# Performance work log

Measured on AMD Instinct MI355X. Metric: run time of the kernel, lower is better.

## Reference

```python
import jax, jax.numpy as jnp
import numpy as np

B, S, D = 2, 4096, 1024
H, HD = 16, 64
M = 512              # memseqlen == chunk size
L = 2 * M            # memory + chunk tokens
HID = 2816
EPS = 1e-5


def setup_inputs() -> dict:
    key = jax.random.key(0)
    ks = jax.random.split(key, 16)
    sc = 0.02
    return {
        "x": jax.random.normal(ks[0], (B, S, D), jnp.float32),
        "freqs_cos": jax.random.uniform(ks[1], (L, HD // 2), jnp.float32),
        "freqs_sin": jax.random.uniform(ks[2], (L, HD // 2), jnp.float32),
        "wq": jax.random.normal(ks[3], (D, D), jnp.float32) * sc,
        "wk": jax.random.normal(ks[4], (D, D), jnp.float32) * sc,
        "wv": jax.random.normal(ks[5], (D, D), jnp.float32) * sc,
        "wo": jax.random.normal(ks[6], (D, D), jnp.float32) * sc,
        "wm": jax.random.normal(ks[7], (D, D), jnp.float32) * sc,
        "wkm": jax.random.normal(ks[8], (D, D), jnp.float32) * sc,
        "wvm": jax.random.normal(ks[9], (D, D), jnp.float32) * sc,
        "w1": jax.random.normal(ks[10], (D, HID), jnp.float32) * sc,
        "w3": jax.random.normal(ks[11], (D, HID), jnp.float32) * sc,
        "w2": jax.random.normal(ks[12], (HID, D), jnp.float32) * sc,
        "ffn_norm_w": jnp.ones((D,), jnp.float32),
        "mem_norm_w": jnp.ones((D,), jnp.float32),
        "origin_mem": jnp.zeros((1, M, D), jnp.float32),
    }


def _rmsnorm(x, w):
    return x * jax.lax.rsqrt(jnp.mean(x * x, axis=-1, keepdims=True) + EPS) * w


def _rope(t, cos, sin):
    # t: (B, L, H, HD); cos/sin: (L, HD//2). Adjacent-pair complex rotation (llama2.c style).
    tr = t.reshape(*t.shape[:-1], HD // 2, 2)
    t_r, t_i = tr[..., 0], tr[..., 1]
    c = cos[None, :, None, :]
    s = sin[None, :, None, :]
    o_r = t_r * c - t_i * s
    o_i = t_r * s + t_i * c
    return jnp.stack([o_r, o_i], axis=-1).reshape(t.shape)


def reference(x, freqs_cos, freqs_sin, wq, wk, wv, wo, wm, wkm, wvm,
              w1, w2, w3, ffn_norm_w, mem_norm_w, origin_mem):
    bsz = x.shape[0]
    cos = freqs_cos[:L]
    sin = freqs_sin[:L]
    causal = jnp.tril(jnp.ones((L, L), dtype=bool))
    scale = 1.0 / jnp.sqrt(jnp.asarray(HD, x.dtype))

    def ffn(h):
        return (jax.nn.silu(h @ w1) * (h @ w3)) @ w2

    def step(om, subx):
        # token projections
        xq = (subx @ wq).reshape(bsz, M, H, HD)
        xk = (subx @ wk).reshape(bsz, M, H, HD)
        xv = (subx @ wv).reshape(bsz, M, H, HD)
        # memory glue: wm -> ffn residual -> rmsnorm
        om2 = om @ wm
        om2 = om2 + ffn(_rmsnorm(om2, ffn_norm_w))
        om2 = _rmsnorm(om2, mem_norm_w)
        # memory projections (source bug: mq is overwritten by mk; wqm unused)
        mk = (om2 @ wkm).reshape(bsz, M, H, HD)
        mv = (om2 @ wvm).reshape(bsz, M, H, HD)
        mq = mk
        q = jnp.concatenate([mq, xq], axis=1)  # (B, L, H, HD)
        k = jnp.concatenate([mk, xk], axis=1)
        v = jnp.concatenate([mv, xv], axis=1)
        q = _rope(q, cos, sin)
        k = _rope(k, cos, sin)
        # SDPA, causal over the concatenated length (n_rep == 1, repeat_kv is identity)
        qh = q.transpose(0, 2, 1, 3)
        kh = k.transpose(0, 2, 1, 3)
        vh = v.transpose(0, 2, 1, 3)
        scores = jnp.einsum('bhqd,bhkd->bhqk', qh, kh) * scale
        scores = jnp.where(causal, scores, jnp.finfo(scores.dtype).min)
        attn = jax.nn.softmax(scores, axis=-1)
        out = jnp.einsum('bhqk,bhkd->bhqd', attn, vh)
        out = out.transpose(0, 2, 1, 3).reshape(bsz, L, D)
        om_new = out[:, M:]  # token-part becomes next memory AND this chunk's output
        return om_new, om_new

    om0 = jnp.broadcast_to(origin_mem, (bsz, M, D))
    xc = x.reshape(bsz, S // M, M, D).transpose(1, 0, 2, 3)  # (n_chunks, B, M, D)
    _, outs = jax.lax.scan(step, om0, xc)
    out = outs.transpose(1, 0, 2, 3).reshape(bsz, S, D)
    return out @ wo
```

## Files before the change

kernel.cpp:

```cpp
#include <hip/hip_runtime.h>
#include <hip/hip_bf16.h>


#define D_    1024
#define H_    16
#define HD_   64
#define M_    512
#define L_    1024
#define HID_  2816
#define NSTEP 8

typedef __hip_bfloat16 bf16;
typedef _Float16 f16;
typedef __attribute__((ext_vector_type(8))) short short8;
typedef __attribute__((ext_vector_type(8))) _Float16 f16x8;
typedef __attribute__((ext_vector_type(2))) _Float16 f16x2;
typedef __attribute__((ext_vector_type(4))) float floatx4;

__global__ void probe_dtype(const void* x, int* flag) {
  int lane = threadIdx.x;
  unsigned short v = ((const unsigned short*)x)[2 * lane];
  int e = (v >> 7) & 0xFF;
  bool sane = (e >= 100 && e <= 140);
  unsigned long long m = __ballot(sane);
  if (lane == 0) flag[0] = (__popcll(m) >= 40) ? 1 : 0;
}

__device__ __forceinline__ float load_any(const void* p, long i, int isbf) {
  return isbf ? __bfloat162float(((const bf16*)p)[i]) : ((const float*)p)[i];
}

__global__ __launch_bounds__(256) void transpose_cast(const void* in, bf16* out,
                                                      int K, int N, const int* flagp,
                                                      int stride, int off) {
  __shared__ float tile[32][33];
  int isbf = flagp[0];
  int tx = threadIdx.x & 31, ty = threadIdx.x >> 5;
  int n = blockIdx.x * 32 + tx;
#pragma unroll
  for (int i = 0; i < 4; i++) {
    int k = blockIdx.y * 32 + ty + i * 8;
    tile[ty + i * 8][tx] = load_any(in, (long)k * N + n, isbf);
  }
  __syncthreads();
  int k2 = blockIdx.y * 32 + tx;
#pragma unroll
  for (int i = 0; i < 4; i++) {
    int n2 = blockIdx.x * 32 + ty + i * 8;
    out[((long)n2 * stride + off) * K + k2] = __float2bfloat16(tile[tx][ty + i * 8]);
  }
}

__global__ __launch_bounds__(256) void cast_to_bf16(const void* in, bf16* out, int n,
                                                    const int* flagp) {
  int i = blockIdx.x * 256 + threadIdx.x;
  if (i < n) out[i] = __float2bfloat16(load_any(in, i, flagp[0]));
}

__global__ __launch_bounds__(256) void cast_to_f32(const void* in, float* out, int n,
                                                   const int* flagp) {
  int i = blockIdx.x * 256 + threadIdx.x;
  if (i < n) out[i] = load_any(in, i, flagp[0]);
}

__global__ __launch_bounds__(256) void init_om(const void* in, bf16* om, const int* flagp) {
  int i = blockIdx.x * 256 + threadIdx.x;
  int rem = i & (M_ * D_ - 1);
  om[i] = __float2bfloat16(load_any(in, rem, flagp[0]));
}

#define GEMM64_BODY(Aptr, WTptr, Kld, kbeg, kend)                                   \
  __shared__ char smem[16384];                                                      \
  char* aT = smem;                                                                  \
  char* bT = smem + 8192;                                                           \
  int tid = threadIdx.x;                                                            \
  int wave = tid >> 6, lane = tid & 63;                                             \
  int wm_ = wave >> 1, wn_ = wave & 1;                                              \
  floatx4 acc[2][2] = {};                                                           \
  int q0 = tid, q1 = tid + 256;                                                     \
  int am0 = q0 >> 3, ac0 = q0 & 7;                                                  \
  int am1 = q1 >> 3, ac1 = q1 & 7;                                                  \
  long grow0 = R0 + am0, grow1 = R0 + am1;                                          \
  long bn0 = (long)(C0 + am0) * (Kld), bn1 = (long)(C0 + am1) * (Kld);              \
  int lofa0 = (am0 * 8 + (ac0 ^ (am0 & 7))) * 16;                                   \
  int lofa1 = (am1 * 8 + (ac1 ^ (am1 & 7))) * 16;                                   \
  for (int k0 = (kbeg); k0 < (kend); k0 += 64) {                                    \
    uint4 va0 = *(const uint4*)((Aptr) + grow0 * (Kld) + k0 + ac0 * 8);             \
    uint4 va1 = *(const uint4*)((Aptr) + grow1 * (Kld) + k0 + ac1 * 8);             \
    uint4 vb0 = *(const uint4*)((WTptr) + bn0 + k0 + ac0 * 8);                      \
    uint4 vb1 = *(const uint4*)((WTptr) + bn1 + k0 + ac1 * 8);                      \
    __syncthreads();                                                                \
    *(uint4*)(aT + lofa0) = va0;                                                    \
    *(uint4*)(aT + lofa1) = va1;                                                    \
    *(uint4*)(bT + lofa0) = vb0;                                                    \
    *(uint4*)(bT + lofa1) = vb1;                                                    \
    __syncthreads();                                                                \
    _Pragma("unroll") for (int kki = 0; kki < 2; ++kki) {                           \
      int cbase = kki * 4 + (lane >> 4);                                            \
      short8 af[2], bfr[2];                                                         \
      _Pragma("unroll") for (int i = 0; i < 2; ++i) {                               \
        int ml = wm_ * 32 + i * 16 + (lane & 15);                                   \
        af[i] = *(const short8*)(aT + (ml * 8 + (cbase ^ (ml & 7))) * 16);          \
        int nl = wn_ * 32 + i * 16 + (lane & 15);                                   \
        bfr[i] = *(const short8*)(bT + (nl * 8 + (cbase ^ (nl & 7))) * 16);         \
      }                                                                             \
      _Pragma("unroll") for (int i = 0; i < 2; ++i)                                 \
          _Pragma("unroll") for (int j = 0; j < 2; ++j) acc[i][j] =                 \
              __builtin_amdgcn_mfma_f32_16x16x32_bf16(af[i], bfr[j], acc[i][j],     \
                                                      0, 0, 0);                     \
    }                                                                               \
  }

__global__ __launch_bounds__(256) void gemm64(
    const bf16* __restrict__ A, const bf16* __restrict__ WT,
    void* __restrict__ out, const int* __restrict__ flagp,
    int N, int K, int out_mode) {
  int C0 = blockIdx.x * 64, R0 = blockIdx.y * 64;
  GEMM64_BODY(A, WT, K, 0, K)
  int isbf = flagp[0];
#pragma unroll
  for (int i = 0; i < 2; ++i)
#pragma unroll
    for (int j = 0; j < 2; ++j) {
      int row = R0 + wm_ * 32 + i * 16 + (lane >> 4) * 4;
      int col = C0 + wn_ * 32 + j * 16 + (lane & 15);
#pragma unroll
      for (int rg = 0; rg < 4; ++rg) {
        float v = acc[i][j][rg];
        long off = (long)(row + rg) * N + col;
        if (out_mode == 0) ((float*)out)[off] = v;
        else if (out_mode == 1) ((f16*)out)[off] = (f16)v;
        else {
          if (isbf) ((bf16*)out)[off] = __float2bfloat16(v);
          else ((float*)out)[off] = v;
        }
      }
    }
}

__global__ __launch_bounds__(256) void gemm64_sk(
    const bf16* __restrict__ A, const bf16* __restrict__ WT,
    float* __restrict__ out0, float* __restrict__ out1,
    int N, int Kfull, int Ksplit) {
  int C0 = blockIdx.x * 64, R0 = blockIdx.y * 64;
  int kb = blockIdx.z;
  float* out = kb ? out1 : out0;
  int kbeg = kb * Ksplit;
  GEMM64_BODY(A, WT, Kfull, kbeg, kbeg + Ksplit)
#pragma unroll
  for (int i = 0; i < 2; ++i)
#pragma unroll
    for (int j = 0; j < 2; ++j) {
      int row = R0 + wm_ * 32 + i * 16 + (lane >> 4) * 4;
      int col = C0 + wn_ * 32 + j * 16 + (lane & 15);
#pragma unroll
      for (int rg = 0; rg < 4; ++rg)
        out[(long)(row + rg) * N + col] = acc[i][j][rg];
    }
}

__global__ __launch_bounds__(256) void gemm64_kmvm(
    const bf16* __restrict__ A, const bf16* __restrict__ WT,
    const float* __restrict__ cosf, const float* __restrict__ sinf,
    f16* __restrict__ k_mem, f16* __restrict__ v_memT) {
  int C0 = blockIdx.x * 64, R0 = blockIdx.y * 64;
  GEMM64_BODY(A, WT, 1024, 0, 1024)
#pragma unroll
  for (int i = 0; i < 2; ++i)
#pragma unroll
    for (int j = 0; j < 2; ++j) {
      int row0 = R0 + wm_ * 32 + i * 16 + (lane >> 4) * 4;
      int col = C0 + wn_ * 32 + j * 16 + (lane & 15);
#pragma unroll
      for (int rg = 0; rg < 4; ++rg) {
        float v = acc[i][j][rg];
        int row = row0 + rg;
        int b = row >> 9, pos = row & 511;
        if (C0 < 1024) {
          float partner = __shfl_xor(v, 1);
          int ii = (col & 63) >> 1;
          float c = cosf[pos * 32 + ii], s = sinf[pos * 32 + ii];
          float o = (col & 1) ? (partner * s + v * c) : (v * c - partner * s);
          int bh = b * 16 + ((col >> 6) & 15);
          k_mem[((size_t)bh * 512 + pos) * 64 + (col & 63)] = (f16)o;
        } else {
          int d = col & 63;
          int bh = b * 16 + ((col - 1024) >> 6);
          v_memT[((size_t)bh * 64 + d) * 512 + pos] = (f16)v;
        }
      }
    }
}

__global__ __launch_bounds__(256) void gemm128(
    const bf16* __restrict__ A, const bf16* __restrict__ WT,
    void* __restrict__ out, const int* __restrict__ flagp,
    int N, int K, int out_mode) {
  __shared__ char smem[32768];
  int tid = threadIdx.x;
  int w = tid >> 6, lane = tid & 63;
  int bx = blockIdx.x, by = blockIdx.y;
  {
    int nwg = gridDim.x * gridDim.y;
    if ((nwg & 7) == 0) {
      int lin = by * gridDim.x + bx;
      int swz = (lin & 7) * (nwg >> 3) + (lin >> 3);
      bx = swz % gridDim.x;
      by = swz / gridDim.x;
    }
  }
  int C0 = bx * 128, R0 = by * 128;
  int wm = (w >> 1) * 64, wn = (w & 1) * 64;
  int g = lane >> 4, n16 = lane & 15;
  floatx4 acc[4][4] = {};
  int lr = lane >> 3, lc = lane & 7;

  for (int k0 = 0; k0 < K; k0 += 64) {
    __syncthreads();
#pragma unroll
    for (int i = 0; i < 4; ++i) {
      int m = w * 32 + i * 8 + lr;
      int cg = lc ^ (m & 7);
      const bf16* ga = A + (size_t)(R0 + m) * K + k0 + cg * 8;
      const bf16* gb = WT + (size_t)(C0 + m) * K + k0 + cg * 8;
      __builtin_amdgcn_global_load_lds(
          (const __attribute__((address_space(1))) void*)ga,
          (__attribute__((address_space(3))) void*)(smem + (w * 32 + i * 8) * 128),
          16, 0, 0);
      __builtin_amdgcn_global_load_lds(
          (const __attribute__((address_space(1))) void*)gb,
          (__attribute__((address_space(3))) void*)(smem + 16384 + (w * 32 + i * 8) * 128),
          16, 0, 0);
    }
    __syncthreads();
#pragma unroll
    for (int kk = 0; kk < 2; ++kk) {
      short8 af[4], bfr[4];
#pragma unroll
      for (int i = 0; i < 4; ++i) {
        int ml = wm + i * 16 + n16;
        af[i] = *(const short8*)(smem + (ml * 8 + ((kk * 4 + g) ^ (ml & 7))) * 16);
        int nl = wn + i * 16 + n16;
        bfr[i] = *(const short8*)(smem + 16384 + (nl * 8 + ((kk * 4 + g) ^ (nl & 7))) * 16);
      }
#pragma unroll
      for (int i = 0; i < 4; ++i)
#pragma unroll
        for (int j = 0; j < 4; ++j)
          acc[i][j] = __builtin_amdgcn_mfma_f32_16x16x32_bf16(af[i], bfr[j], acc[i][j], 0, 0, 0);
    }
  }
  int isbf = flagp[0];
#pragma unroll
  for (int i = 0; i < 4; ++i)
#pragma unroll
    for (int j = 0; j < 4; ++j) {
      int row = R0 + wm + i * 16 + g * 4;
      int col = C0 + wn + j * 16 + n16;
#pragma unroll
      for (int rg = 0; rg < 4; ++rg) {
        float v = acc[i][j][rg];
        if (out_mode == 3) {
          float partner = __shfl_xor(v, 1);
          if ((n16 & 1) == 0) {
            float a = v;
            float s = a / (1.f + __expf(-a));
            ((bf16*)out)[(long)(row + rg) * HID_ + (col >> 1)] =
                __float2bfloat16(s * partner);
          }
          continue;
        }
        long off = (long)(row + rg) * N + col;
        if (out_mode == 0) ((float*)out)[off] = v;
        else if (out_mode == 1) ((f16*)out)[off] = (f16)v;
        else {
          if (isbf) ((bf16*)out)[off] = __float2bfloat16(v);
          else ((float*)out)[off] = v;
        }
      }
    }
}

__global__ __launch_bounds__(256) void rmsnorm_cast(const float* __restrict__ X,
                                                    const float* __restrict__ Wn,
                                                    bf16* __restrict__ Y,
                                                    const float* __restrict__ X1,
                                                    const float* __restrict__ X2,
                                                    float* __restrict__ sumout) {
  int row = blockIdx.x, tid = threadIdx.x;
  const float* xr = X + (long)row * D_;
  float vals[4], ss = 0.f;
#pragma unroll
  for (int i = 0; i < 4; i++) {
    int c = tid + i * 256;
    float v = xr[c];
    if (X1) v += X1[(long)row * D_ + c];
    if (X2) v += X2[(long)row * D_ + c];
    vals[i] = v;
    ss += v * v;
  }
#pragma unroll
  for (int off = 32; off; off >>= 1) ss += __shfl_xor(ss, off);
  __shared__ float wsum[4];
  int wv = tid >> 6, lane = tid & 63;
  if (lane == 0) wsum[wv] = ss;
  __syncthreads();
  ss = wsum[0] + wsum[1] + wsum[2] + wsum[3];
  float r = rsqrtf(ss * (1.0f / D_) + 1e-5f);
#pragma unroll
  for (int i = 0; i < 4; i++) {
    int c = tid + i * 256;
    if (sumout) sumout[(long)row * D_ + c] = vals[i];
    Y[(long)row * D_ + c] = __float2bfloat16(vals[i] * r * Wn[c]);
  }
}

__global__ __launch_bounds__(256) void rope_x(
    const f16* __restrict__ qkv, const float* __restrict__ cosf,
    const float* __restrict__ sinf, f16* __restrict__ q_x,
    f16* __restrict__ k_x, f16* __restrict__ v_xT) {
  __shared__ f16 tile[64][72];
  int pt = blockIdx.x;
  int t = blockIdx.y;
  int bh = blockIdx.z;
  int b = bh >> 4, h = bh & 15;
  int tid = threadIdx.x;
  int i = tid & 31, p0 = tid >> 5;
  size_t slab = (size_t)t * 32 + bh;
#pragma unroll
  for (int j = 0; j < 8; ++j) {
    int pl = p0 + j * 8;
    int m = pt * 64 + pl;
    int pos = 512 + m;
    long base = ((long)b * 4096 + t * 512 + m) * 3072 + h * 64 + 2 * i;
    float c = cosf[pos * 32 + i], s = sinf[pos * 32 + i];
    float q0 = (float)qkv[base], q1 = (float)qkv[base + 1];
    f16x2 qw; qw.x = (f16)((q0 * c - q1 * s) * 0.125f);
    qw.y = (f16)((q0 * s + q1 * c) * 0.125f);
    *(f16x2*)(q_x + (slab * 512 + m) * 64 + 2 * i) = qw;
    float k0 = (float)qkv[base + 1024], k1 = (float)qkv[base + 1025];
    f16x2 kw; kw.x = (f16)(k0 * c - k1 * s); kw.y = (f16)(k0 * s + k1 * c);
    *(f16x2*)(k_x + (slab * 512 + m) * 64 + 2 * i) = kw;
    tile[2 * i][pl] = qkv[base + 2048];
    tile[2 * i + 1][pl] = qkv[base + 2049];
  }
  __syncthreads();
#pragma unroll
  for (int j = 0; j < 8; ++j) {
    int d = p0 + j * 8;
    f16x2 vv; vv.x = tile[d][2 * i]; vv.y = tile[d][2 * i + 1];
    *(f16x2*)(v_xT + (slab * 64 + d) * 512 + pt * 64 + 2 * i) = vv;
  }
}

__global__ __launch_bounds__(256) void attn_mfma(
    const f16* __restrict__ q_x, const f16* __restrict__ k_mem,
    const f16* __restrict__ v_memT, const f16* __restrict__ k_x,
    const f16* __restrict__ v_xT, float* __restrict__ Opart,
    float* __restrict__ mpart, float* __restrict__ lpart, int t) {
  __shared__ char smem[24576];
  int qt = blockIdx.x, bh = blockIdx.y, z = blockIdx.z;
  int tid = threadIdx.x;
  int w = tid >> 6, lane = tid & 63;
  int g = lane >> 4, n16 = lane & 15;
  int c0 = z ? 8 : 0;
  int numc = z ? (qt + 1) : 8;
  int pos = 512 + qt * 64 + w * 16 + n16;
  size_t slab = (size_t)t * 32 + bh;

  f16x8 qf[2];
  {
    const f16* qp = q_x + (slab * 512 + qt * 64 + w * 16 + n16) * 64 + g * 8;
    qf[0] = *(const f16x8*)(qp);
    qf[1] = *(const f16x8*)(qp + 32);
  }
  floatx4 O[4] = {};
  float mrun = -1e30f, lrun = 0.f;

  int id0 = tid, id1 = tid + 256;
  int r0 = id0 >> 3, cc0 = id0 & 7;
  int r1 = id1 >> 3, cc1 = id1 & 7;
  int lof0 = ((r0 << 3) | (cc0 ^ (r0 & 7))) * 16;
  int lof1 = ((r1 << 3) | (cc1 ^ (r1 & 7))) * 16;

  auto kaddr = [&](int c, int r) -> const f16* {
    return (c < 8) ? k_mem + ((size_t)bh * 512 + c * 64 + r) * 64
                   : k_x + (slab * 512 + (c - 8) * 64 + r) * 64;
  };
  auto vaddr = [&](int c, int d) -> const f16* {
    return (c < 8) ? v_memT + ((size_t)bh * 64 + d) * 512 + c * 64
                   : v_xT + (slab * 64 + d) * 512 + (c - 8) * 64;
  };

  uint4 kv0 = *(const uint4*)(kaddr(c0, r0) + cc0 * 8);
  uint4 kv1 = *(const uint4*)(kaddr(c0, r1) + cc1 * 8);
  uint4 vv0 = *(const uint4*)(vaddr(c0, r0) + cc0 * 8);
  uint4 vv1 = *(const uint4*)(vaddr(c0, r1) + cc1 * 8);

  char* Pw = smem + 16384 + w * 2048;

  for (int c = 0; c < numc; ++c) {
    __syncthreads();
    *(uint4*)(smem + lof0) = kv0;
    *(uint4*)(smem + lof1) = kv1;
    *(uint4*)(smem + 8192 + lof0) = vv0;
    *(uint4*)(smem + 8192 + lof1) = vv1;
    if (c + 1 < numc) {
      kv0 = *(const uint4*)(kaddr(c0 + c + 1, r0) + cc0 * 8);
      kv1 = *(const uint4*)(kaddr(c0 + c + 1, r1) + cc1 * 8);
      vv0 = *(const uint4*)(vaddr(c0 + c + 1, r0) + cc0 * 8);
      vv1 = *(const uint4*)(vaddr(c0 + c + 1, r1) + cc1 * 8);
    }
    __syncthreads();

    floatx4 S[4] = {};
    __builtin_amdgcn_s_setprio(1);
#pragma unroll
    for (int kk = 0; kk < 2; ++kk) {
#pragma unroll
      for (int tn = 0; tn < 4; ++tn) {
        int row = tn * 16 + n16;
        f16x8 kf = *(const f16x8*)(smem + (((row << 3) | ((kk * 4 + g) ^ (row & 7))) * 16));
        S[tn] = __builtin_amdgcn_mfma_f32_16x16x32_f16(kf, qf[kk], S[tn], 0, 0, 0);
      }
    }
    __builtin_amdgcn_s_setprio(0);
    if (z == 1 && c == numc - 1) {
      int kb = 512 + qt * 64;
#pragma unroll
      for (int tn = 0; tn < 4; ++tn)
#pragma unroll
        for (int r = 0; r < 4; ++r) {
          int key = kb + tn * 16 + g * 4 + r;
          if (key > pos) S[tn][r] = -1e30f;
        }
    }
    float smax = -1e30f;
#pragma unroll
    for (int tn = 0; tn < 4; ++tn)
#pragma unroll
      for (int r = 0; r < 4; ++r) smax = fmaxf(smax, S[tn][r]);
    smax = fmaxf(smax, __shfl_xor(smax, 16));
    smax = fmaxf(smax, __shfl_xor(smax, 32));
    float newm = fmaxf(mrun, smax);
    float corr = __expf(mrun - newm);
    mrun = newm;
    float lsum = 0.f;
    f16 pv[16];
#pragma unroll
    for (int tn = 0; tn < 4; ++tn)
#pragma unroll
      for (int r = 0; r < 4; ++r) {
        float p = __expf(S[tn][r] - newm);
        lsum += p;
        pv[tn * 4 + r] = (f16)p;
      }
    lsum += __shfl_xor(lsum, 16);
    lsum += __shfl_xor(lsum, 32);
    lrun = lrun * corr + lsum;
    float cr[4];
#pragma unroll
    for (int r = 0; r < 4; ++r) cr[r] = __shfl(corr, g * 4 + r);
#pragma unroll
    for (int dt = 0; dt < 4; ++dt)
#pragma unroll
      for (int r = 0; r < 4; ++r) O[dt][r] *= cr[r];
#pragma unroll
    for (int tn = 0; tn < 4; ++tn)
#pragma unroll
      for (int r = 0; r < 4; ++r) {
        int kap = tn * 16 + g * 4 + r;
        *(f16*)(Pw + (((n16 << 3) | ((kap >> 3) ^ (n16 & 7))) * 16 + (kap & 7) * 2)) =
            pv[tn * 4 + r];
      }
    __builtin_amdgcn_s_setprio(1);
#pragma unroll
    for (int kk = 0; kk < 2; ++kk) {
      f16x8 pf = *(const f16x8*)(Pw + (((n16 << 3) | ((kk * 4 + g) ^ (n16 & 7))) * 16));
#pragma unroll
      for (int dt = 0; dt < 4; ++dt) {
        int row = dt * 16 + n16;
        f16x8 vf =
            *(const f16x8*)(smem + 8192 + (((row << 3) | ((kk * 4 + g) ^ (row & 7))) * 16));
        O[dt] = __builtin_amdgcn_mfma_f32_16x16x32_f16(pf, vf, O[dt], 0, 0, 0);
      }
    }
    __builtin_amdgcn_s_setprio(0);
  }
  int b = bh >> 4, h = bh & 15;
  if (g == 0) {
    int qq = qt * 64 + w * 16 + n16;
    mpart[(size_t)z * 16384 + bh * 512 + qq] = mrun;
    lpart[(size_t)z * 16384 + bh * 512 + qq] = lrun;
  }
#pragma unroll
  for (int dt = 0; dt < 4; ++dt)
#pragma unroll
    for (int r = 0; r < 4; ++r) {
      int qq = qt * 64 + w * 16 + g * 4 + r;
      size_t col = (size_t)h * 64 + dt * 16 + n16;
      Opart[(size_t)z * 1048576 + (size_t)(b * 512 + qq) * 1024 + col] = O[dt][r];
    }
}

__global__ __launch_bounds__(256) void attn_merge(
    const float* __restrict__ Opart, const float* __restrict__ mpart,
    const float* __restrict__ lpart, bf16* __restrict__ om_bf,
    bf16* __restrict__ outs_bf, int t) {
  int row = blockIdx.x;
  int b = row >> 9, qq = row & 511;
  int tid = threadIdx.x;
#pragma unroll
  for (int ii = 0; ii < 4; ++ii) {
    int col = tid + ii * 256;
    int bh = b * 16 + (col >> 6);
    int idx = bh * 512 + qq;
    float m1 = mpart[idx], l1 = lpart[idx];
    float m2 = mpart[16384 + idx], l2 = lpart[16384 + idx];
    float Mx = fmaxf(m1, m2);
    float a1 = __expf(m1 - Mx), a2 = __expf(m2 - Mx);
    float o1 = Opart[(size_t)row * 1024 + col];
    float o2 = Opart[1048576 + (size_t)row * 1024 + col];
    float v = (a1 * o1 + a2 * o2) / (a1 * l1 + a2 * l2);
    bf16 bv = __float2bfloat16(v);
    om_bf[(size_t)row * 1024 + col] = bv;
    outs_bf[((size_t)(b * 4096 + t * 512 + qq)) * 1024 + col] = bv;
  }
}

extern "C" void kernel_launch(void* const* d_in, const int* in_sizes, int n_in,
                              void* d_out, int out_size, void* d_ws, size_t ws_size,
                              hipStream_t stream) {
  (void)in_sizes; (void)n_in; (void)out_size; (void)ws_size;
  const void* x   = d_in[0];
  const void* fc  = d_in[1];
  const void* fs  = d_in[2];
  const void* wq  = d_in[3];
  const void* wk  = d_in[4];
  const void* wv  = d_in[5];
  const void* wo  = d_in[6];
  const void* wm  = d_in[7];
  const void* wkm = d_in[8];
  const void* wvm = d_in[9];
  const void* w1  = d_in[10];
  const void* w3  = d_in[11];
  const void* w2  = d_in[12];
  const void* fnw = d_in[13];
  const void* mnw = d_in[14];
  const void* om0 = d_in[15];

  char* p = (char*)d_ws;
  auto alloc = [&](size_t bytes) -> char* {
    char* r = p;
    p += (bytes + 255) & ~(size_t)255;
    return r;
  };
  int*   flag    = (int*)alloc(256);
  bf16*  wqkvT   = (bf16*)alloc((size_t)3 * 1048576 * 2);
  bf16*  wmT     = (bf16*)alloc((size_t)1048576 * 2);
  bf16*  wkmvmT  = (bf16*)alloc((size_t)2 * 1048576 * 2);
  bf16*  w13T    = (bf16*)alloc((size_t)2 * 2883584 * 2);
  bf16*  w2T     = (bf16*)alloc((size_t)2883584 * 2);
  bf16*  woT     = (bf16*)alloc((size_t)1048576 * 2);
  bf16*  xb      = (bf16*)alloc((size_t)8388608 * 2);
  float* cosf    = (float*)alloc((size_t)32768 * 4);
  float* sinf    = (float*)alloc((size_t)32768 * 4);
  float* ffnw    = (float*)alloc((size_t)1024 * 4);
  float* memw    = (float*)alloc((size_t)1024 * 4);
  bf16*  om_bf   = (bf16*)alloc((size_t)1048576 * 2);
  bf16*  outs_bf = (bf16*)alloc((size_t)8388608 * 2);
  f16*   q_x     = (f16*)alloc((size_t)8 * 32 * 512 * 64 * 2);
  f16*   k_x     = (f16*)alloc((size_t)8 * 32 * 512 * 64 * 2);
  f16*   v_xT    = (f16*)alloc((size_t)8 * 32 * 512 * 64 * 2);
  char*  shr     = alloc((size_t)8192 * 3072 * 2);
  f16*   qkvf_all = (f16*)shr;
  char*  lp = shr;
  auto lalloc = [&](size_t bytes) -> char* {
    char* r = lp;
    lp += (bytes + 255) & ~(size_t)255;
    return r;
  };
  float* om2a   = (float*)lalloc((size_t)1048576 * 4);
  bf16*  h_bf   = (bf16*)lalloc((size_t)1048576 * 2);
  bf16*  u_bf   = (bf16*)lalloc((size_t)2883584 * 2);
  float* fbuf   = (float*)lalloc((size_t)1048576 * 4);
  float* fbuf2  = (float*)lalloc((size_t)1048576 * 4);
  bf16*  om2_bf = (bf16*)lalloc((size_t)1048576 * 2);
  f16*   k_mem  = (f16*)lalloc((size_t)1048576 * 2);
  f16*   v_memT = (f16*)lalloc((size_t)1048576 * 2);
  float* Opart  = (float*)lalloc((size_t)2 * 1048576 * 4);
  float* mpart  = (float*)lalloc((size_t)2 * 16384 * 4);
  float* lpart  = (float*)lalloc((size_t)2 * 16384 * 4);

  dim3 tb(256);
  probe_dtype<<<1, 64, 0, stream>>>(x, flag);

  transpose_cast<<<dim3(32, 32), tb, 0, stream>>>(wq, wqkvT, 1024, 1024, flag, 1, 0);
  transpose_cast<<<dim3(32, 32), tb, 0, stream>>>(wk, wqkvT + 1048576, 1024, 1024, flag, 1, 0);
  transpose_cast<<<dim3(32, 32), tb, 0, stream>>>(wv, wqkvT + 2 * 1048576, 1024, 1024, flag, 1, 0);
  transpose_cast<<<dim3(32, 32), tb, 0, stream>>>(wm, wmT, 1024, 1024, flag, 1, 0);
  transpose_cast<<<dim3(32, 32), tb, 0, stream>>>(wkm, wkmvmT, 1024, 1024, flag, 1, 0);
  transpose_cast<<<dim3(32, 32), tb, 0, stream>>>(wvm, wkmvmT + 1048576, 1024, 1024, flag, 1, 0);
  transpose_cast<<<dim3(88, 32), tb, 0, stream>>>(w1, w13T, 1024, 2816, flag, 2, 0);
  transpose_cast<<<dim3(88, 32), tb, 0, stream>>>(w3, w13T, 1024, 2816, flag, 2, 1);
  transpose_cast<<<dim3(32, 88), tb, 0, stream>>>(w2, w2T, 2816, 1024, flag, 1, 0);
  transpose_cast<<<dim3(32, 32), tb, 0, stream>>>(wo, woT, 1024, 1024, flag, 1, 0);

  cast_to_bf16<<<32768, tb, 0, stream>>>(x, xb, 8388608, flag);
  cast_to_f32<<<128, tb, 0, stream>>>(fc, cosf, 32768, flag);
  cast_to_f32<<<128, tb, 0, stream>>>(fs, sinf, 32768, flag);
  cast_to_f32<<<4, tb, 0, stream>>>(fnw, ffnw, 1024, flag);
  cast_to_f32<<<4, tb, 0, stream>>>(mnw, memw, 1024, flag);
  init_om<<<4096, tb, 0, stream>>>(om0, om_bf, flag);

  gemm128<<<dim3(24, 64), tb, 0, stream>>>(xb, wqkvT, qkvf_all, flag, 3072, 1024, 1);
  rope_x<<<dim3(8, 8, 32), tb, 0, stream>>>(qkvf_all, cosf, sinf, q_x, k_x, v_xT);

  for (int t = 0; t < NSTEP; ++t) {
    gemm64_sk<<<dim3(16, 16, 2), tb, 0, stream>>>(om_bf, wmT, om2a, fbuf, 1024, 1024, 512);
    rmsnorm_cast<<<1024, tb, 0, stream>>>(om2a, ffnw, h_bf, fbuf, nullptr, om2a);
    gemm128<<<dim3(44, 8), tb, 0, stream>>>(h_bf, w13T, u_bf, flag, 5632, 1024, 3);
    gemm64_sk<<<dim3(16, 16, 2), tb, 0, stream>>>(u_bf, w2T, fbuf, fbuf2, 1024, 2816, 1408);
    rmsnorm_cast<<<1024, tb, 0, stream>>>(om2a, memw, om2_bf, fbuf, fbuf2, nullptr);
    gemm64_kmvm<<<dim3(32, 16), tb, 0, stream>>>(om2_bf, wkmvmT, cosf, sinf, k_mem, v_memT);
    attn_mfma<<<dim3(8, 32, 2), tb, 0, stream>>>(q_x, k_mem, v_memT, k_x, v_xT,
                                                 Opart, mpart, lpart, t);
    attn_merge<<<1024, tb, 0, stream>>>(Opart, mpart, lpart, om_bf, outs_bf, t);
  }
  gemm128<<<dim3(8, 64), tb, 0, stream>>>(outs_bf, woT, d_out, flag, 1024, 1024, 2);
}
```

Before: 1.140 ms.

## Widen attention key tiles to 128 and split the w2 GEMM four ways

The attention kernel now stages two 64-key chunks (128 keys) per iteration in 48 KB of LDS, with wider score and probability tiles. This halves the loop trips, syncs and softmax rescales. The w2 split-K GEMM goes from 2 to 4 K-partitions written into one strided partial buffer, and rmsnorm_cast sums a variable number of partials. The gemm128 XCD-aware block swizzle is removed and the unused gemm64 kernel is deleted. Risks: lower occupancy from more LDS and registers in attention, and a possibly masked over-read past the last chunk when the chunk count is odd.

```diff
diff --git a/kernel.cpp b/kernel.cpp
--- a/kernel.cpp
+++ b/kernel.cpp
@@ -111,40 +111,12 @@
     }                                                                               \
   }
 
-__global__ __launch_bounds__(256) void gemm64(
-    const bf16* __restrict__ A, const bf16* __restrict__ WT,
-    void* __restrict__ out, const int* __restrict__ flagp,
-    int N, int K, int out_mode) {
-  int C0 = blockIdx.x * 64, R0 = blockIdx.y * 64;
-  GEMM64_BODY(A, WT, K, 0, K)
-  int isbf = flagp[0];
-#pragma unroll
-  for (int i = 0; i < 2; ++i)
-#pragma unroll
-    for (int j = 0; j < 2; ++j) {
-      int row = R0 + wm_ * 32 + i * 16 + (lane >> 4) * 4;
-      int col = C0 + wn_ * 32 + j * 16 + (lane & 15);
-#pragma unroll
-      for (int rg = 0; rg < 4; ++rg) {
-        float v = acc[i][j][rg];
-        long off = (long)(row + rg) * N + col;
-        if (out_mode == 0) ((float*)out)[off] = v;
-        else if (out_mode == 1) ((f16*)out)[off] = (f16)v;
-        else {
-          if (isbf) ((bf16*)out)[off] = __float2bfloat16(v);
-          else ((float*)out)[off] = v;
-        }
-      }
-    }
-}
-
 __global__ __launch_bounds__(256) void gemm64_sk(
     const bf16* __restrict__ A, const bf16* __restrict__ WT,
-    float* __restrict__ out0, float* __restrict__ out1,
-    int N, int Kfull, int Ksplit) {
+    float* __restrict__ outP, int N, int Kfull, int Ksplit) {
   int C0 = blockIdx.x * 64, R0 = blockIdx.y * 64;
   int kb = blockIdx.z;
-  float* out = kb ? out1 : out0;
+  float* out = outP + ((size_t)kb << 20);
   int kbeg = kb * Ksplit;
   GEMM64_BODY(A, WT, Kfull, kbeg, kbeg + Ksplit)
 #pragma unroll
@@ -199,17 +171,7 @@
   __shared__ char smem[32768];
   int tid = threadIdx.x;
   int w = tid >> 6, lane = tid & 63;
-  int bx = blockIdx.x, by = blockIdx.y;
-  {
-    int nwg = gridDim.x * gridDim.y;
-    if ((nwg & 7) == 0) {
-      int lin = by * gridDim.x + bx;
-      int swz = (lin & 7) * (nwg >> 3) + (lin >> 3);
-      bx = swz % gridDim.x;
-      by = swz / gridDim.x;
-    }
-  }
-  int C0 = bx * 128, R0 = by * 128;
+  int C0 = blockIdx.x * 128, R0 = blockIdx.y * 128;
   int wm = (w >> 1) * 64, wn = (w & 1) * 64;
   int g = lane >> 4, n16 = lane & 15;
   floatx4 acc[4][4] = {};
@@ -284,18 +246,17 @@
 __global__ __launch_bounds__(256) void rmsnorm_cast(const float* __restrict__ X,
                                                     const float* __restrict__ Wn,
                                                     bf16* __restrict__ Y,
-                                                    const float* __restrict__ X1,
-                                                    const float* __restrict__ X2,
+                                                    const float* __restrict__ P,
+                                                    int np,
                                                     float* __restrict__ sumout) {
   int row = blockIdx.x, tid = threadIdx.x;
-  const float* xr = X + (long)row * D_;
   float vals[4], ss = 0.f;
 #pragma unroll
   for (int i = 0; i < 4; i++) {
     int c = tid + i * 256;
-    float v = xr[c];
-    if (X1) v += X1[(long)row * D_ + c];
-    if (X2) v += X2[(long)row * D_ + c];
+    long idx = (long)row * D_ + c;
+    float v = X ? X[idx] : 0.f;
+    for (int k = 0; k < np; ++k) v += P[((size_t)k << 20) + idx];
     vals[i] = v;
     ss += v * v;
   }
@@ -358,13 +319,14 @@
     const f16* __restrict__ v_memT, const f16* __restrict__ k_x,
     const f16* __restrict__ v_xT, float* __restrict__ Opart,
     float* __restrict__ mpart, float* __restrict__ lpart, int t) {
-  __shared__ char smem[24576];
+  __shared__ char smem[49152];
   int qt = blockIdx.x, bh = blockIdx.y, z = blockIdx.z;
   int tid = threadIdx.x;
   int w = tid >> 6, lane = tid & 63;
   int g = lane >> 4, n16 = lane & 15;
   int c0 = z ? 8 : 0;
   int numc = z ? (qt + 1) : 8;
+  int niter = (numc + 1) >> 1;
   int pos = 512 + qt * 64 + w * 16 + n16;
   size_t slab = (size_t)t * 32 + bh;
 
@@ -376,12 +338,6 @@
   }
   floatx4 O[4] = {};
   float mrun = -1e30f, lrun = 0.f;
-
-  int id0 = tid, id1 = tid + 256;
-  int r0 = id0 >> 3, cc0 = id0 & 7;
-  int r1 = id1 >> 3, cc1 = id1 & 7;
-  int lof0 = ((r0 << 3) | (cc0 ^ (r0 & 7))) * 16;
-  int lof1 = ((r1 << 3) | (cc1 ^ (r1 & 7))) * 16;
 
   auto kaddr = [&](int c, int r) -> const f16* {
     return (c < 8) ? k_mem + ((size_t)bh * 512 + c * 64 + r) * 64
@@ -392,43 +348,57 @@
                    : v_xT + (slab * 64 + d) * 512 + (c - 8) * 64;
   };
 
-  uint4 kv0 = *(const uint4*)(kaddr(c0, r0) + cc0 * 8);
-  uint4 kv1 = *(const uint4*)(kaddr(c0, r1) + cc1 * 8);
-  uint4 vv0 = *(const uint4*)(vaddr(c0, r0) + cc0 * 8);
-  uint4 vv1 = *(const uint4*)(vaddr(c0, r1) + cc1 * 8);
-
-  char* Pw = smem + 16384 + w * 2048;
-
-  for (int c = 0; c < numc; ++c) {
+  int ksr[4], ksc[4], vsr[4], vsc[4], kLof[4], vLof[4];
+#pragma unroll
+  for (int j = 0; j < 4; ++j) {
+    int s = tid + 256 * j;
+    ksr[j] = s >> 3; ksc[j] = s & 7;
+    vsr[j] = s >> 4; vsc[j] = s & 15;
+    kLof[j] = (ksr[j] * 8 + (ksc[j] ^ (ksr[j] & 7))) * 16;
+    vLof[j] = (vsr[j] * 16 + (vsc[j] ^ (vsr[j] & 15))) * 16;
+  }
+  uint4 kvr[4], vvr[4];
+#pragma unroll
+  for (int j = 0; j < 4; ++j) {
+    kvr[j] = *(const uint4*)(kaddr(c0, ksr[j]) + ksc[j] * 8);
+    vvr[j] = *(const uint4*)(vaddr(c0, vsr[j]) + vsc[j] * 8);
+  }
+
+  char* Pw = smem + 32768 + w * 4096;
+
+  for (int it = 0; it < niter; ++it) {
     __syncthreads();
-    *(uint4*)(smem + lof0) = kv0;
-    *(uint4*)(smem + lof1) = kv1;
-    *(uint4*)(smem + 8192 + lof0) = vv0;
-    *(uint4*)(smem + 8192 + lof1) = vv1;
-    if (c + 1 < numc) {
-      kv0 = *(const uint4*)(kaddr(c0 + c + 1, r0) + cc0 * 8);
-      kv1 = *(const uint4*)(kaddr(c0 + c + 1, r1) + cc1 * 8);
-      vv0 = *(const uint4*)(vaddr(c0 + c + 1, r0) + cc0 * 8);
-      vv1 = *(const uint4*)(vaddr(c0 + c + 1, r1) + cc1 * 8);
+#pragma unroll
+    for (int j = 0; j < 4; ++j) {
+      *(uint4*)(smem + kLof[j]) = kvr[j];
+      *(uint4*)(smem + 16384 + vLof[j]) = vvr[j];
+    }
+    if (it + 1 < niter) {
+      int ca = c0 + 2 * (it + 1);
+#pragma unroll
+      for (int j = 0; j < 4; ++j) {
+        kvr[j] = *(const uint4*)(kaddr(ca, ksr[j]) + ksc[j] * 8);
+        vvr[j] = *(const uint4*)(vaddr(ca, vsr[j]) + vsc[j] * 8);
+      }
     }
     __syncthreads();
 
-    floatx4 S[4] = {};
+    floatx4 S[8] = {};
     __builtin_amdgcn_s_setprio(1);
 #pragma unroll
     for (int kk = 0; kk < 2; ++kk) {
 #pragma unroll
-      for (int tn = 0; tn < 4; ++tn) {
+      for (int tn = 0; tn < 8; ++tn) {
         int row = tn * 16 + n16;
-        f16x8 kf = *(const f16x8*)(smem + (((row << 3) | ((kk * 4 + g) ^ (row & 7))) * 16));
+        f16x8 kf = *(const f16x8*)(smem + (row * 8 + ((kk * 4 + g) ^ (row & 7))) * 16);
         S[tn] = __builtin_amdgcn_mfma_f32_16x16x32_f16(kf, qf[kk], S[tn], 0, 0, 0);
       }
     }
     __builtin_amdgcn_s_setprio(0);
-    if (z == 1 && c == numc - 1) {
-      int kb = 512 + qt * 64;
-#pragma unroll
-      for (int tn = 0; tn < 4; ++tn)
+    if (z == 1 && it == niter - 1) {
+      int kb = 512 + 2 * it * 64;
+#pragma unroll
+      for (int tn = 0; tn < 8; ++tn)
 #pragma unroll
         for (int r = 0; r < 4; ++r) {
           int key = kb + tn * 16 + g * 4 + r;
@@ -437,7 +407,7 @@
     }
     float smax = -1e30f;
 #pragma unroll
-    for (int tn = 0; tn < 4; ++tn)
+    for (int tn = 0; tn < 8; ++tn)
 #pragma unroll
       for (int r = 0; r < 4; ++r) smax = fmaxf(smax, S[tn][r]);
     smax = fmaxf(smax, __shfl_xor(smax, 16));
@@ -446,9 +416,9 @@
     float corr = __expf(mrun - newm);
     mrun = newm;
     float lsum = 0.f;
-    f16 pv[16];
-#pragma unroll
-    for (int tn = 0; tn < 4; ++tn)
+    f16 pv[32];
+#pragma unroll
+    for (int tn = 0; tn < 8; ++tn)
 #pragma unroll
       for (int r = 0; r < 4; ++r) {
         float p = __expf(S[tn][r] - newm);
@@ -466,22 +436,22 @@
 #pragma unroll
       for (int r = 0; r < 4; ++r) O[dt][r] *= cr[r];
 #pragma unroll
-    for (int tn = 0; tn < 4; ++tn)
+    for (int tn = 0; tn < 8; ++tn)
 #pragma unroll
       for (int r = 0; r < 4; ++r) {
         int kap = tn * 16 + g * 4 + r;
-        *(f16*)(Pw + (((n16 << 3) | ((kap >> 3) ^ (n16 & 7))) * 16 + (kap & 7) * 2)) =
+        *(f16*)(Pw + (n16 * 16 + ((kap >> 3) ^ n16)) * 16 + (kap & 7) * 2) =
             pv[tn * 4 + r];
       }
     __builtin_amdgcn_s_setprio(1);
 #pragma unroll
-    for (int kk = 0; kk < 2; ++kk) {
-      f16x8 pf = *(const f16x8*)(Pw + (((n16 << 3) | ((kk * 4 + g) ^ (n16 & 7))) * 16));
+    for (int kk = 0; kk < 4; ++kk) {
+      f16x8 pf = *(const f16x8*)(Pw + (n16 * 16 + ((kk * 4 + g) ^ n16)) * 16);
 #pragma unroll
       for (int dt = 0; dt < 4; ++dt) {
         int row = dt * 16 + n16;
-        f16x8 vf =
-            *(const f16x8*)(smem + 8192 + (((row << 3) | ((kk * 4 + g) ^ (row & 7))) * 16));
+        f16x8 vf = *(const f16x8*)(smem + 16384 +
+                                   (row * 16 + ((kk * 4 + g) ^ (row & 15))) * 16);
         O[dt] = __builtin_amdgcn_mfma_f32_16x16x32_f16(pf, vf, O[dt], 0, 0, 0);
       }
     }
@@ -583,8 +553,7 @@
   float* om2a   = (float*)lalloc((size_t)1048576 * 4);
   bf16*  h_bf   = (bf16*)lalloc((size_t)1048576 * 2);
   bf16*  u_bf   = (bf16*)lalloc((size_t)2883584 * 2);
-  float* fbuf   = (float*)lalloc((size_t)1048576 * 4);
-  float* fbuf2  = (float*)lalloc((size_t)1048576 * 4);
+  float* om2P   = (float*)lalloc((size_t)4 * 1048576 * 4);
   bf16*  om2_bf = (bf16*)lalloc((size_t)1048576 * 2);
   f16*   k_mem  = (f16*)lalloc((size_t)1048576 * 2);
   f16*   v_memT = (f16*)lalloc((size_t)1048576 * 2);
@@ -617,11 +586,11 @@
   rope_x<<<dim3(8, 8, 32), tb, 0, stream>>>(qkvf_all, cosf, sinf, q_x, k_x, v_xT);
 
   for (int t = 0; t < NSTEP; ++t) {
-    gemm64_sk<<<dim3(16, 16, 2), tb, 0, stream>>>(om_bf, wmT, om2a, fbuf, 1024, 1024, 512);
-    rmsnorm_cast<<<1024, tb, 0, stream>>>(om2a, ffnw, h_bf, fbuf, nullptr, om2a);
+    gemm64_sk<<<dim3(16, 16, 2), tb, 0, stream>>>(om_bf, wmT, om2P, 1024, 1024, 512);
+    rmsnorm_cast<<<1024, tb, 0, stream>>>(nullptr, ffnw, h_bf, om2P, 2, om2a);
     gemm128<<<dim3(44, 8), tb, 0, stream>>>(h_bf, w13T, u_bf, flag, 5632, 1024, 3);
-    gemm64_sk<<<dim3(16, 16, 2), tb, 0, stream>>>(u_bf, w2T, fbuf, fbuf2, 1024, 2816, 1408);
-    rmsnorm_cast<<<1024, tb, 0, stream>>>(om2a, memw, om2_bf, fbuf, fbuf2, nullptr);
+    gemm64_sk<<<dim3(16, 16, 4), tb, 0, stream>>>(u_bf, w2T, om2P, 1024, 2816, 704);
+    rmsnorm_cast<<<1024, tb, 0, stream>>>(om2a, memw, om2_bf, om2P, 4, nullptr);
     gemm64_kmvm<<<dim3(32, 16), tb, 0, stream>>>(om2_bf, wkmvmT, cosf, sinf, k_mem, v_memT);
     attn_mfma<<<dim3(8, 32, 2), tb, 0, stream>>>(q_x, k_mem, v_memT, k_x, v_xT,
                                                  Opart, mpart, lpart, t);
```

After: 1.263 ms. 1.11x slower.

## Fuse RoPE and QKV layout scatter into projection GEMM epilogue

Applied to the files above, without the earlier changes.

Adds an epilogue mode to the 128-tile GEMM that applies RoPE and the query scale to the Q/K columns and writes the V columns transposed. This removes the separate rope_x kernel and the f16 QKV intermediate round trip. It also removes the workgroup-index swizzle in gemm128, which may hurt L2 locality. The split-K partial buffers are merged into one strided buffer consumed by rmsnorm_cast, and buffers are no longer aliased in a shared arena. The fused epilogue uses scattered 2-byte stores for Q/K, which could be less coalesced.

```diff
diff --git a/kernel.cpp b/kernel.cpp
--- a/kernel.cpp
+++ b/kernel.cpp
@@ -14,6 +14,7 @@
 typedef _Float16 f16;
 typedef __attribute__((ext_vector_type(8))) short short8;
 typedef __attribute__((ext_vector_type(8))) _Float16 f16x8;
+typedef __attribute__((ext_vector_type(4))) _Float16 f16x4;
 typedef __attribute__((ext_vector_type(2))) _Float16 f16x2;
 typedef __attribute__((ext_vector_type(4))) float floatx4;
 
@@ -111,40 +112,12 @@
     }                                                                               \
   }
 
-__global__ __launch_bounds__(256) void gemm64(
-    const bf16* __restrict__ A, const bf16* __restrict__ WT,
-    void* __restrict__ out, const int* __restrict__ flagp,
-    int N, int K, int out_mode) {
-  int C0 = blockIdx.x * 64, R0 = blockIdx.y * 64;
-  GEMM64_BODY(A, WT, K, 0, K)
-  int isbf = flagp[0];
-#pragma unroll
-  for (int i = 0; i < 2; ++i)
-#pragma unroll
-    for (int j = 0; j < 2; ++j) {
-      int row = R0 + wm_ * 32 + i * 16 + (lane >> 4) * 4;
-      int col = C0 + wn_ * 32 + j * 16 + (lane & 15);
-#pragma unroll
-      for (int rg = 0; rg < 4; ++rg) {
-        float v = acc[i][j][rg];
-        long off = (long)(row + rg) * N + col;
-        if (out_mode == 0) ((float*)out)[off] = v;
-        else if (out_mode == 1) ((f16*)out)[off] = (f16)v;
-        else {
-          if (isbf) ((bf16*)out)[off] = __float2bfloat16(v);
-          else ((float*)out)[off] = v;
-        }
-      }
-    }
-}
-
 __global__ __launch_bounds__(256) void gemm64_sk(
     const bf16* __restrict__ A, const bf16* __restrict__ WT,
-    float* __restrict__ out0, float* __restrict__ out1,
-    int N, int Kfull, int Ksplit) {
+    float* __restrict__ outP, int N, int Kfull, int Ksplit) {
   int C0 = blockIdx.x * 64, R0 = blockIdx.y * 64;
   int kb = blockIdx.z;
-  float* out = kb ? out1 : out0;
+  float* out = outP + ((size_t)kb << 20);
   int kbeg = kb * Ksplit;
   GEMM64_BODY(A, WT, Kfull, kbeg, kbeg + Ksplit)
 #pragma unroll
@@ -195,21 +168,13 @@
 __global__ __launch_bounds__(256) void gemm128(
     const bf16* __restrict__ A, const bf16* __restrict__ WT,
     void* __restrict__ out, const int* __restrict__ flagp,
-    int N, int K, int out_mode) {
+    int N, int K, int out_mode,
+    const float* __restrict__ cosf, const float* __restrict__ sinf,
+    f16* __restrict__ q_x, f16* __restrict__ k_x, f16* __restrict__ v_xT) {
   __shared__ char smem[32768];
   int tid = threadIdx.x;
   int w = tid >> 6, lane = tid & 63;
-  int bx = blockIdx.x, by = blockIdx.y;
-  {
-    int nwg = gridDim.x * gridDim.y;
-    if ((nwg & 7) == 0) {
-      int lin = by * gridDim.x + bx;
-      int swz = (lin & 7) * (nwg >> 3) + (lin >> 3);
-      bx = swz % gridDim.x;
-      by = swz / gridDim.x;
-    }
-  }
-  int C0 = bx * 128, R0 = by * 128;
+  int C0 = blockIdx.x * 128, R0 = blockIdx.y * 128;
   int wm = (w >> 1) * 64, wn = (w & 1) * 64;
   int g = lane >> 4, n16 = lane & 15;
   floatx4 acc[4][4] = {};
@@ -250,13 +215,44 @@
           acc[i][j] = __builtin_amdgcn_mfma_f32_16x16x32_bf16(af[i], bfr[j], acc[i][j], 0, 0, 0);
     }
   }
-  int isbf = flagp[0];
+  int isbf = flagp ? flagp[0] : 0;
 #pragma unroll
   for (int i = 0; i < 4; ++i)
 #pragma unroll
     for (int j = 0; j < 4; ++j) {
       int row = R0 + wm + i * 16 + g * 4;
       int col = C0 + wn + j * 16 + n16;
+      if (out_mode == 4) {
+        if (col < 2048) {
+#pragma unroll
+          for (int rg = 0; rg < 4; ++rg) {
+            float v = acc[i][j][rg];
+            float partner = __shfl_xor(v, 1);
+            int r = row + rg;
+            int m = r & 511, t = (r >> 9) & 7, b = r >> 12;
+            int pos = 512 + m;
+            int ii = (col & 63) >> 1;
+            float c = cosf[pos * 32 + ii], s = sinf[pos * 32 + ii];
+            float o = (col & 1) ? (partner * s + v * c) : (v * c - partner * s);
+            int h = (col >> 6) & 15;
+            size_t slab = (size_t)t * 32 + b * 16 + h;
+            if (col < 1024)
+              q_x[(slab * 512 + m) * 64 + (col & 63)] = (f16)(o * 0.125f);
+            else
+              k_x[(slab * 512 + m) * 64 + (col & 63)] = (f16)o;
+          }
+        } else {
+          int r = row;
+          int m = r & 511, t = (r >> 9) & 7, b = r >> 12;
+          int d = col & 63, h = (col - 2048) >> 6;
+          size_t slab = (size_t)t * 32 + b * 16 + h;
+          f16x4 vv;
+#pragma unroll
+          for (int rg = 0; rg < 4; ++rg) vv[rg] = (f16)acc[i][j][rg];
+          *(f16x4*)(v_xT + (slab * 64 + d) * 512 + m) = vv;
+        }
+        continue;
+      }
 #pragma unroll
       for (int rg = 0; rg < 4; ++rg) {
         float v = acc[i][j][rg];
@@ -284,18 +280,17 @@
 __global__ __launch_bounds__(256) void rmsnorm_cast(const float* __restrict__ X,
                                                     const float* __restrict__ Wn,
                                                     bf16* __restrict__ Y,
-                                                    const float* __restrict__ X1,
-                                                    const float* __restrict__ X2,
+                                                    const float* __restrict__ P,
+                                                    int np,
                                                     float* __restrict__ sumout) {
   int row = blockIdx.x, tid = threadIdx.x;
-  const float* xr = X + (long)row * D_;
   float vals[4], ss = 0.f;
 #pragma unroll
   for (int i = 0; i < 4; i++) {
     int c = tid + i * 256;
-    float v = xr[c];
-    if (X1) v += X1[(long)row * D_ + c];
-    if (X2) v += X2[(long)row * D_ + c];
+    long idx = (long)row * D_ + c;
+    float v = X ? X[idx] : 0.f;
+    for (int k = 0; k < np; ++k) v += P[((size_t)k << 20) + idx];
     vals[i] = v;
     ss += v * v;
   }
@@ -312,44 +307,6 @@
     int c = tid + i * 256;
     if (sumout) sumout[(long)row * D_ + c] = vals[i];
     Y[(long)row * D_ + c] = __float2bfloat16(vals[i] * r * Wn[c]);
-  }
-}
-
-__global__ __launch_bounds__(256) void rope_x(
-    const f16* __restrict__ qkv, const float* __restrict__ cosf,
-    const float* __restrict__ sinf, f16* __restrict__ q_x,
-    f16* __restrict__ k_x, f16* __restrict__ v_xT) {
-  __shared__ f16 tile[64][72];
-  int pt = blockIdx.x;
-  int t = blockIdx.y;
-  int bh = blockIdx.z;
-  int b = bh >> 4, h = bh & 15;
-  int tid = threadIdx.x;
-  int i = tid & 31, p0 = tid >> 5;
-  size_t slab = (size_t)t * 32 + bh;
-#pragma unroll
-  for (int j = 0; j < 8; ++j) {
-    int pl = p0 + j * 8;
-    int m = pt * 64 + pl;
-    int pos = 512 + m;
-    long base = ((long)b * 4096 + t * 512 + m) * 3072 + h * 64 + 2 * i;
-    float c = cosf[pos * 32 + i], s = sinf[pos * 32 + i];
-    float q0 = (float)qkv[base], q1 = (float)qkv[base + 1];
-    f16x2 qw; qw.x = (f16)((q0 * c - q1 * s) * 0.125f);
-    qw.y = (f16)((q0 * s + q1 * c) * 0.125f);
-    *(f16x2*)(q_x + (slab * 512 + m) * 64 + 2 * i) = qw;
-    float k0 = (float)qkv[base + 1024], k1 = (float)qkv[base + 1025];
-    f16x2 kw; kw.x = (f16)(k0 * c - k1 * s); kw.y = (f16)(k0 * s + k1 * c);
-    *(f16x2*)(k_x + (slab * 512 + m) * 64 + 2 * i) = kw;
-    tile[2 * i][pl] = qkv[base + 2048];
-    tile[2 * i + 1][pl] = qkv[base + 2049];
-  }
-  __syncthreads();
-#pragma unroll
-  for (int j = 0; j < 8; ++j) {
-    int d = p0 + j * 8;
-    f16x2 vv; vv.x = tile[d][2 * i]; vv.y = tile[d][2 * i + 1];
-    *(f16x2*)(v_xT + (slab * 64 + d) * 512 + pt * 64 + 2 * i) = vv;
   }
 }
 
@@ -572,25 +529,16 @@
   f16*   q_x     = (f16*)alloc((size_t)8 * 32 * 512 * 64 * 2);
   f16*   k_x     = (f16*)alloc((size_t)8 * 32 * 512 * 64 * 2);
   f16*   v_xT    = (f16*)alloc((size_t)8 * 32 * 512 * 64 * 2);
-  char*  shr     = alloc((size_t)8192 * 3072 * 2);
-  f16*   qkvf_all = (f16*)shr;
-  char*  lp = shr;
-  auto lalloc = [&](size_t bytes) -> char* {
-    char* r = lp;
-    lp += (bytes + 255) & ~(size_t)255;
-    return r;
-  };
-  float* om2a   = (float*)lalloc((size_t)1048576 * 4);
-  bf16*  h_bf   = (bf16*)lalloc((size_t)1048576 * 2);
-  bf16*  u_bf   = (bf16*)lalloc((size_t)2883584 * 2);
-  float* fbuf   = (float*)lalloc((size_t)1048576 * 4);
-  float* fbuf2  = (float*)lalloc((size_t)1048576 * 4);
-  bf16*  om2_bf = (bf16*)lalloc((size_t)1048576 * 2);
-  f16*   k_mem  = (f16*)lalloc((size_t)1048576 * 2);
-  f16*   v_memT = (f16*)lalloc((size_t)1048576 * 2);
-  float* Opart  = (float*)lalloc((size_t)2 * 1048576 * 4);
-  float* mpart  = (float*)lalloc((size_t)2 * 16384 * 4);
-  float* lpart  = (float*)lalloc((size_t)2 * 16384 * 4);
+  float* om2a   = (float*)alloc((size_t)1048576 * 4);
+  bf16*  h_bf   = (bf16*)alloc((size_t)1048576 * 2);
+  bf16*  u_bf   = (bf16*)alloc((size_t)2883584 * 2);
+  float* om2P   = (float*)alloc((size_t)2 * 1048576 * 4);
+  bf16*  om2_bf = (bf16*)alloc((size_t)1048576 * 2);
+  f16*   k_mem  = (f16*)alloc((size_t)1048576 * 2);
+  f16*   v_memT = (f16*)alloc((size_t)1048576 * 2);
+  float* Opart  = (float*)alloc((size_t)2 * 1048576 * 4);
+  float* mpart  = (float*)alloc((size_t)2 * 16384 * 4);
+  float* lpart  = (float*)alloc((size_t)2 * 16384 * 4);
 
   dim3 tb(256);
   probe_dtype<<<1, 64, 0, stream>>>(x, flag);
@@ -613,19 +561,21 @@
   cast_to_f32<<<4, tb, 0, stream>>>(mnw, memw, 1024, flag);
   init_om<<<4096, tb, 0, stream>>>(om0, om_bf, flag);
 
-  gemm128<<<dim3(24, 64), tb, 0, stream>>>(xb, wqkvT, qkvf_all, flag, 3072, 1024, 1);
-  rope_x<<<dim3(8, 8, 32), tb, 0, stream>>>(qkvf_all, cosf, sinf, q_x, k_x, v_xT);
+  gemm128<<<dim3(24, 64), tb, 0, stream>>>(xb, wqkvT, nullptr, flag, 3072, 1024, 4,
+                                           cosf, sinf, q_x, k_x, v_xT);
 
   for (int t = 0; t < NSTEP; ++t) {
-    gemm64_sk<<<dim3(16, 16, 2), tb, 0, stream>>>(om_bf, wmT, om2a, fbuf, 1024, 1024, 512);
-    rmsnorm_cast<<<1024, tb, 0, stream>>>(om2a, ffnw, h_bf, fbuf, nullptr, om2a);
-    gemm128<<<dim3(44, 8), tb, 0, stream>>>(h_bf, w13T, u_bf, flag, 5632, 1024, 3);
-    gemm64_sk<<<dim3(16, 16, 2), tb, 0, stream>>>(u_bf, w2T, fbuf, fbuf2, 1024, 2816, 1408);
-    rmsnorm_cast<<<1024, tb, 0, stream>>>(om2a, memw, om2_bf, fbuf, fbuf2, nullptr);
+    gemm64_sk<<<dim3(16, 16, 2), tb, 0, stream>>>(om_bf, wmT, om2P, 1024, 1024, 512);
+    rmsnorm_cast<<<1024, tb, 0, stream>>>(nullptr, ffnw, h_bf, om2P, 2, om2a);
+    gemm128<<<dim3(44, 8), tb, 0, stream>>>(h_bf, w13T, u_bf, flag, 5632, 1024, 3,
+                                            nullptr, nullptr, nullptr, nullptr, nullptr);
+    gemm64_sk<<<dim3(16, 16, 2), tb, 0, stream>>>(u_bf, w2T, om2P, 1024, 2816, 1408);
+    rmsnorm_cast<<<1024, tb, 0, stream>>>(om2a, memw, om2_bf, om2P, 2, nullptr);
     gemm64_kmvm<<<dim3(32, 16), tb, 0, stream>>>(om2_bf, wkmvmT, cosf, sinf, k_mem, v_memT);
     attn_mfma<<<dim3(8, 32, 2), tb, 0, stream>>>(q_x, k_mem, v_memT, k_x, v_xT,
                                                  Opart, mpart, lpart, t);
     attn_merge<<<1024, tb, 0, stream>>>(Opart, mpart, lpart, om_bf, outs_bf, t);
   }
-  gemm128<<<dim3(8, 64), tb, 0, stream>>>(outs_bf, woT, d_out, flag, 1024, 1024, 2);
-}
+  gemm128<<<dim3(8, 64), tb, 0, stream>>>(outs_bf, woT, d_out, flag, 1024, 1024, 2,
+                                          nullptr, nullptr, nullptr, nullptr, nullptr);
+}
```

Result: no change. 1.132 ms (-0.7%).
